# Performance work log

Hardware: AMD Instinct MI355X
Metric: run time of the kernel (lower is better)

Reference implementation:

```python
import jax, jax.numpy as jnp
import numpy as np

LATENT = 3
POLY = 3
SINDY_DIM = 22  # 3 ones + 3 linear + 6 quad + 10 cubic


def sindy_library(z, poly_order=POLY, latent_dim=LATENT):
    # z: [N, latent_dim] -> [N, sindy_dim]; mirrors the torch loop ordering.
    N = z.shape[0]
    cols = [jnp.ones((N,), z.dtype) for _ in range(latent_dim)]
    if poly_order > 0:
        cols += [z[:, i] for i in range(latent_dim)]
    if poly_order > 1:
        for i in range(latent_dim):
            for j in range(i, latent_dim):
                cols.append(z[:, i] * z[:, j])
    if poly_order > 2:
        for i in range(latent_dim):
            for j in range(i, latent_dim):
                for k in range(j, latent_dim):
                    cols.append(z[:, i] * z[:, j] * z[:, k])
    return jnp.stack(cols, axis=1)


def _xavier(key, out_f, in_f):
    lim = np.sqrt(6.0 / (in_f + out_f)).astype(np.float32)
    return jax.random.uniform(key, (out_f, in_f), jnp.float32, -lim, lim)


def setup_inputs() -> dict:
    key = jax.random.key(0)
    ks = jax.random.split(key, 16)
    N, D = 262144, 128
    we = [128, 64, 32, 3]
    wd = [3, 32, 64, 128]
    d = {}
    d["x"] = jax.random.normal(ks[0], (N, D), jnp.float32)
    d["dx"] = jax.random.normal(ks[1], (N, D), jnp.float32)
    for li, (i_f, o_f) in enumerate(zip(we[:-1], we[1:])):
        d[f"We{li+1}"] = _xavier(ks[2 + li], o_f, i_f)
        d[f"be{li+1}"] = jnp.zeros((o_f,), jnp.float32)
    for li, (i_f, o_f) in enumerate(zip(wd[:-1], wd[1:])):
        d[f"Wd{li+1}"] = _xavier(ks[6 + li], o_f, i_f)
        d[f"bd{li+1}"] = jnp.zeros((o_f,), jnp.float32)
    d["EW"] = jnp.full((LATENT, SINDY_DIM), 0.5, jnp.float32)  # nn.init.constant_(E.weight, 0.5)
    d["Eb"] = jax.random.normal(ks[10], (LATENT,), jnp.float32) * 0.1
    return d


def reference(x, dx, We1, be1, We2, be2, We3, be3,
              Wd1, bd1, Wd2, bd2, Wd3, bd3, EW, Eb):
    # encoder forward (Linear + Identity chain)
    z = ((x @ We1.T + be1) @ We2.T + be2) @ We3.T + be3            # [N, L]
    # encoder Jacobian is constant (pure linear chain): J_enc = We3 @ We2 @ We1
    J_enc = We3 @ We2 @ We1                                        # [L, D]
    dz = dx @ J_enc.T                                              # [N, L]
    # SINDy prediction of z-dot
    theta = sindy_library(z)                                       # [N, SINDY_DIM]
    dzb = theta @ EW.T + Eb                                        # [N, L]
    # decoder forward
    xb = ((z @ Wd1.T + bd1) @ Wd2.T + bd2) @ Wd3.T + bd3           # [N, D]
    # decoder Jacobian (constant)
    J_dec = Wd3 @ Wd2 @ Wd1                                        # [D, L]
    dxb = dzb @ J_dec.T                                            # [N, D]
    return z, dz, dzb, xb, dxb
```

## Files before the change

### kernel.cpp

```cpp
#include <hip/hip_runtime.h>

#define D 128

typedef float f32x4 __attribute__((ext_vector_type(4)));

__global__ __launch_bounds__(256) void fuse_weights(
    const float* __restrict__ We1, const float* __restrict__ be1,
    const float* __restrict__ We2, const float* __restrict__ be2,
    const float* __restrict__ We3, const float* __restrict__ be3,
    const float* __restrict__ Wd1, const float* __restrict__ bd1,
    const float* __restrict__ Wd2, const float* __restrict__ bd2,
    const float* __restrict__ Wd3, const float* __restrict__ bd3,
    float* __restrict__ ws)
{
    __shared__ float A1[3][64];
    __shared__ float B1[64][3];
    __shared__ float t2d[64];
    const int t = threadIdx.x;

    if (t < 192) {
        {   int r = t >> 6, c = t & 63;
            float s = 0.f;
            #pragma unroll 8
            for (int i = 0; i < 32; ++i) s += We3[r * 32 + i] * We2[i * 64 + c];
            A1[r][c] = s;
        }
        {   int o = t / 3, l = t - o * 3;
            float s = 0.f;
            #pragma unroll 8
            for (int i = 0; i < 32; ++i) s += Wd2[o * 32 + i] * Wd1[i * 3 + l];
            B1[o][l] = s;
        }
    } else {
        int i = t - 192;
        float s = bd2[i];
        #pragma unroll 8
        for (int j = 0; j < 32; ++j) s += Wd2[i * 32 + j] * bd1[j];
        t2d[i] = s;
    }
    __syncthreads();

    for (int e = t; e < 3 * D; e += 256) {
        int r = e >> 7, c = e & 127;
        float s = 0.f;
        #pragma unroll 8
        for (int j = 0; j < 64; ++j) s += A1[r][j] * We1[j * D + c];
        ws[e] = s;
    }
    if (t < 3) {
        float s = be3[t];
        #pragma unroll 8
        for (int j = 0; j < 64; ++j) s += A1[t][j] * be1[j];
        #pragma unroll 8
        for (int i = 0; i < 32; ++i) s += We3[t * 32 + i] * be2[i];
        ws[384 + t] = s;
    }
    if (t < 128) {
        float s0 = 0.f, s1 = 0.f, s2 = 0.f, sb = bd3[t];
        #pragma unroll 8
        for (int j = 0; j < 64; ++j) {
            float w = Wd3[t * 64 + j];
            s0 += w * B1[j][0];
            s1 += w * B1[j][1];
            s2 += w * B1[j][2];
            sb += w * t2d[j];
        }
        ws[512 + t * 4 + 0] = s0;
        ws[512 + t * 4 + 1] = s1;
        ws[512 + t * 4 + 2] = s2;
        ws[512 + t * 4 + 3] = sb;
    }
}

__global__ __launch_bounds__(256) void enc2(
    const float* __restrict__ x, const float* __restrict__ dx,
    const float* __restrict__ ws, float* __restrict__ zout,
    float* __restrict__ dzout, int nrows)
{
    const int lane = threadIdx.x & 31;
    const int half = threadIdx.x >> 5;

    const f32x4 je0 = *((const f32x4*)(ws + 0 * D) + lane);
    const f32x4 je1 = *((const f32x4*)(ws + 1 * D) + lane);
    const f32x4 je2 = *((const f32x4*)(ws + 2 * D) + lane);
    const float benc0 = ws[384], benc1 = ws[385], benc2 = ws[386];

    const int base = blockIdx.x * 128;

    #pragma unroll 4
    for (int i = 0; i < 16; ++i) {
        const int row = base + i * 8 + half;
        if (row >= nrows) continue;
        const f32x4 xv = __builtin_nontemporal_load((const f32x4*)(x + (size_t)row * D) + lane);
        float z0 = je0.x*xv.x + je0.y*xv.y + je0.z*xv.z + je0.w*xv.w;
        float z1 = je1.x*xv.x + je1.y*xv.y + je1.z*xv.z + je1.w*xv.w;
        float z2 = je2.x*xv.x + je2.y*xv.y + je2.z*xv.z + je2.w*xv.w;
        #pragma unroll
        for (int m = 16; m >= 1; m >>= 1) {
            z0 += __shfl_xor(z0, m);
            z1 += __shfl_xor(z1, m);
            z2 += __shfl_xor(z2, m);
        }
        if (lane < 3) {
            const float zv = (lane == 0) ? z0 + benc0 : (lane == 1) ? z1 + benc1 : z2 + benc2;
            zout[(size_t)row * 3 + lane] = zv;
        }
    }

    __syncthreads();

    #pragma unroll 4
    for (int i = 0; i < 16; ++i) {
        const int row = base + i * 8 + half;
        if (row >= nrows) continue;
        const f32x4 dv = __builtin_nontemporal_load((const f32x4*)(dx + (size_t)row * D) + lane);
        float d0 = je0.x*dv.x + je0.y*dv.y + je0.z*dv.z + je0.w*dv.w;
        float d1 = je1.x*dv.x + je1.y*dv.y + je1.z*dv.z + je1.w*dv.w;
        float d2 = je2.x*dv.x + je2.y*dv.y + je2.z*dv.z + je2.w*dv.w;
        #pragma unroll
        for (int m = 16; m >= 1; m >>= 1) {
            d0 += __shfl_xor(d0, m);
            d1 += __shfl_xor(d1, m);
            d2 += __shfl_xor(d2, m);
        }
        if (lane < 3) {
            const float dvv = (lane == 0) ? d0 : (lane == 1) ? d1 : d2;
            dzout[(size_t)row * 3 + lane] = dvv;
        }
    }
}

__global__ __launch_bounds__(256) void dec2(
    const float* __restrict__ ws, const float* __restrict__ EW,
    const float* __restrict__ Eb, const float* __restrict__ zin,
    float* __restrict__ dzbout, float* __restrict__ xbout,
    float* __restrict__ dxbout, int nrows)
{
    __shared__ float sdzb[384];

    const int lane = threadIdx.x & 31;
    const int half = threadIdx.x >> 5;

    const f32x4 jd0 = *((const f32x4*)(ws + 512) + lane * 4 + 0);
    const f32x4 jd1 = *((const f32x4*)(ws + 512) + lane * 4 + 1);
    const f32x4 jd2 = *((const f32x4*)(ws + 512) + lane * 4 + 2);
    const f32x4 jd3 = *((const f32x4*)(ws + 512) + lane * 4 + 3);

    float ew0[19], ew1[19], ew2[19];
    #pragma unroll
    for (int k = 0; k < 19; ++k) {
        ew0[k] = EW[ 3 + k];
        ew1[k] = EW[25 + k];
        ew2[k] = EW[47 + k];
    }
    const float bs0 = Eb[0] + EW[ 0] + EW[ 1] + EW[ 2];
    const float bs1 = Eb[1] + EW[22] + EW[23] + EW[24];
    const float bs2 = Eb[2] + EW[44] + EW[45] + EW[46];

    const int base = blockIdx.x * 128;

    #pragma unroll 2
    for (int i = 0; i < 16; ++i) {
        const int r2  = i * 8 + half;
        const int row = base + r2;
        if (row >= nrows) continue;

        const float z0 = zin[(size_t)row * 3 + 0];
        const float z1 = zin[(size_t)row * 3 + 1];
        const float z2 = zin[(size_t)row * 3 + 2];

        const float q00 = z0*z0, q01 = z0*z1, q02 = z0*z2;
        const float q11 = z1*z1, q12 = z1*z2, q22 = z2*z2;
        float th[19];
        th[0]=z0;  th[1]=z1;  th[2]=z2;
        th[3]=q00; th[4]=q01; th[5]=q02; th[6]=q11; th[7]=q12; th[8]=q22;
        th[9]=q00*z0;  th[10]=q00*z1; th[11]=q00*z2;
        th[12]=q11*z0; th[13]=q12*z0; th[14]=q22*z0;
        th[15]=q11*z1; th[16]=q11*z2; th[17]=q22*z1; th[18]=q22*z2;

        float b0 = bs0, b1 = bs1, b2 = bs2;
        #pragma unroll
        for (int k = 0; k < 19; ++k) {
            b0 += ew0[k] * th[k];
            b1 += ew1[k] * th[k];
            b2 += ew2[k] * th[k];
        }

        if (lane < 3) {
            const float bv = (lane == 0) ? b0 : (lane == 1) ? b1 : b2;
            dzbout[(size_t)row * 3 + lane] = bv;
            sdzb[r2 * 3 + lane] = bv;
        }

        f32x4 xbv;
        xbv.x = jd0.x*z0 + jd0.y*z1 + jd0.z*z2 + jd0.w;
        xbv.y = jd1.x*z0 + jd1.y*z1 + jd1.z*z2 + jd1.w;
        xbv.z = jd2.x*z0 + jd2.y*z1 + jd2.z*z2 + jd2.w;
        xbv.w = jd3.x*z0 + jd3.y*z1 + jd3.z*z2 + jd3.w;
        __builtin_nontemporal_store(xbv, (f32x4*)(xbout + (size_t)row * D) + lane);
    }

    __syncthreads();

    #pragma unroll 4
    for (int i = 0; i < 16; ++i) {
        const int r2  = i * 8 + half;
        const int row = base + r2;
        if (row >= nrows) continue;

        const float b0 = sdzb[r2 * 3 + 0];
        const float b1 = sdzb[r2 * 3 + 1];
        const float b2 = sdzb[r2 * 3 + 2];

        f32x4 dxbv;
        dxbv.x = jd0.x*b0 + jd0.y*b1 + jd0.z*b2;
        dxbv.y = jd1.x*b0 + jd1.y*b1 + jd1.z*b2;
        dxbv.z = jd2.x*b0 + jd2.y*b1 + jd2.z*b2;
        dxbv.w = jd3.x*b0 + jd3.y*b1 + jd3.z*b2;
        __builtin_nontemporal_store(dxbv, (f32x4*)(dxbout + (size_t)row * D) + lane);
    }
}

extern "C" void kernel_launch(void* const* d_in, const int* in_sizes, int n_in,
                              void* d_out, int out_size, void* d_ws, size_t ws_size,
                              hipStream_t stream) {
    const float* x   = (const float*)d_in[0];
    const float* dx  = (const float*)d_in[1];
    const float* We1 = (const float*)d_in[2];
    const float* be1 = (const float*)d_in[3];
    const float* We2 = (const float*)d_in[4];
    const float* be2 = (const float*)d_in[5];
    const float* We3 = (const float*)d_in[6];
    const float* be3 = (const float*)d_in[7];
    const float* Wd1 = (const float*)d_in[8];
    const float* bd1 = (const float*)d_in[9];
    const float* Wd2 = (const float*)d_in[10];
    const float* bd2 = (const float*)d_in[11];
    const float* Wd3 = (const float*)d_in[12];
    const float* bd3 = (const float*)d_in[13];
    const float* EW  = (const float*)d_in[14];
    const float* Eb  = (const float*)d_in[15];

    float* ws  = (float*)d_ws;
    float* out = (float*)d_out;
    const int nrows = in_sizes[0] / D;
    const int nblk  = (nrows + 127) / 128;

    fuse_weights<<<1, 256, 0, stream>>>(We1, be1, We2, be2, We3, be3,
                                        Wd1, bd1, Wd2, bd2, Wd3, bd3, ws);

    enc2<<<nblk, 256, 0, stream>>>(x, dx, ws,
                                   out,
                                   out + 3 * (size_t)nrows,
                                   nrows);

    dec2<<<nblk, 256, 0, stream>>>(ws, EW, Eb,
                                   out,
                                   out + 6 * (size_t)nrows,
                                   out + 9 * (size_t)nrows,
                                   out + 137 * (size_t)nrows,
                                   nrows);
}
```

Measured before the change: 121.3 us.

## Fuse encoder and decoder kernels into one row-block kernel staging z in LDS

Merges the encoder and decoder kernels into a single kernel that processes 256 rows per block. z, dz and dzb are staged in shared memory and written out with coalesced vector stores. The SINDy polynomial is computed once per row by one thread instead of redundantly across every lane of a wavefront. This removes a kernel launch and the global round trip of z between kernels. In exchange it uses more shared memory per block, has half as many blocks, and puts a serial dependency between the read phase and the write phase inside each block.

```diff
diff --git a/kernel.cpp b/kernel.cpp
--- a/kernel.cpp
+++ b/kernel.cpp
@@ -72,24 +72,39 @@
     }
 }
 
-__global__ __launch_bounds__(256) void enc2(
+__global__ __launch_bounds__(256) void sindy_all(
     const float* __restrict__ x, const float* __restrict__ dx,
-    const float* __restrict__ ws, float* __restrict__ zout,
-    float* __restrict__ dzout, int nrows)
+    const float* __restrict__ EW, const float* __restrict__ Eb,
+    const float* __restrict__ ws, float* __restrict__ out, int nrows)
 {
-    const int lane = threadIdx.x & 31;
-    const int half = threadIdx.x >> 5;
-
-    const f32x4 je0 = *((const f32x4*)(ws + 0 * D) + lane);
-    const f32x4 je1 = *((const f32x4*)(ws + 1 * D) + lane);
-    const f32x4 je2 = *((const f32x4*)(ws + 2 * D) + lane);
+    __shared__ float sz[768];
+    __shared__ float sdz[768];
+    __shared__ float sdzb[768];
+    __shared__ float sew[69];
+
+    const int t    = threadIdx.x;
+    const int lane = t & 31;
+    const int half = t >> 5;
+
+    if (t < 66) sew[t] = EW[t];
+    else if (t < 69) sew[t] = Eb[t - 66];
+
+    const f32x4 je0 = *((const f32x4*)(ws +   0) + lane);
+    const f32x4 je1 = *((const f32x4*)(ws + 128) + lane);
+    const f32x4 je2 = *((const f32x4*)(ws + 256) + lane);
     const float benc0 = ws[384], benc1 = ws[385], benc2 = ws[386];
-
-    const int base = blockIdx.x * 128;
-
-    #pragma unroll 4
-    for (int i = 0; i < 16; ++i) {
-        const int row = base + i * 8 + half;
+    const f32x4 jd0 = *((const f32x4*)(ws + 512) + lane * 4 + 0);
+    const f32x4 jd1 = *((const f32x4*)(ws + 512) + lane * 4 + 1);
+    const f32x4 jd2 = *((const f32x4*)(ws + 512) + lane * 4 + 2);
+    const f32x4 jd3 = *((const f32x4*)(ws + 512) + lane * 4 + 3);
+
+    const int base = blockIdx.x * 256;
+    const int rem  = nrows - base;
+
+    #pragma unroll 4
+    for (int i = 0; i < 32; ++i) {
+        const int r2  = i * 8 + half;
+        const int row = base + r2;
         if (row >= nrows) continue;
         const f32x4 xv = __builtin_nontemporal_load((const f32x4*)(x + (size_t)row * D) + lane);
         float z0 = je0.x*xv.x + je0.y*xv.y + je0.z*xv.z + je0.w*xv.w;
@@ -101,17 +116,17 @@
             z1 += __shfl_xor(z1, m);
             z2 += __shfl_xor(z2, m);
         }
-        if (lane < 3) {
-            const float zv = (lane == 0) ? z0 + benc0 : (lane == 1) ? z1 + benc1 : z2 + benc2;
-            zout[(size_t)row * 3 + lane] = zv;
-        }
-    }
-
-    __syncthreads();
-
-    #pragma unroll 4
-    for (int i = 0; i < 16; ++i) {
-        const int row = base + i * 8 + half;
+        if (lane == 0) {
+            sz[r2 * 3 + 0] = z0 + benc0;
+            sz[r2 * 3 + 1] = z1 + benc1;
+            sz[r2 * 3 + 2] = z2 + benc2;
+        }
+    }
+
+    #pragma unroll 4
+    for (int i = 0; i < 32; ++i) {
+        const int r2  = i * 8 + half;
+        const int row = base + r2;
         if (row >= nrows) continue;
         const f32x4 dv = __builtin_nontemporal_load((const f32x4*)(dx + (size_t)row * D) + lane);
         float d0 = je0.x*dv.x + je0.y*dv.y + je0.z*dv.z + je0.w*dv.w;
@@ -123,51 +138,19 @@
             d1 += __shfl_xor(d1, m);
             d2 += __shfl_xor(d2, m);
         }
-        if (lane < 3) {
-            const float dvv = (lane == 0) ? d0 : (lane == 1) ? d1 : d2;
-            dzout[(size_t)row * 3 + lane] = dvv;
-        }
-    }
-}
-
-__global__ __launch_bounds__(256) void dec2(
-    const float* __restrict__ ws, const float* __restrict__ EW,
-    const float* __restrict__ Eb, const float* __restrict__ zin,
-    float* __restrict__ dzbout, float* __restrict__ xbout,
-    float* __restrict__ dxbout, int nrows)
-{
-    __shared__ float sdzb[384];
-
-    const int lane = threadIdx.x & 31;
-    const int half = threadIdx.x >> 5;
-
-    const f32x4 jd0 = *((const f32x4*)(ws + 512) + lane * 4 + 0);
-    const f32x4 jd1 = *((const f32x4*)(ws + 512) + lane * 4 + 1);
-    const f32x4 jd2 = *((const f32x4*)(ws + 512) + lane * 4 + 2);
-    const f32x4 jd3 = *((const f32x4*)(ws + 512) + lane * 4 + 3);
-
-    float ew0[19], ew1[19], ew2[19];
-    #pragma unroll
-    for (int k = 0; k < 19; ++k) {
-        ew0[k] = EW[ 3 + k];
-        ew1[k] = EW[25 + k];
-        ew2[k] = EW[47 + k];
-    }
-    const float bs0 = Eb[0] + EW[ 0] + EW[ 1] + EW[ 2];
-    const float bs1 = Eb[1] + EW[22] + EW[23] + EW[24];
-    const float bs2 = Eb[2] + EW[44] + EW[45] + EW[46];
-
-    const int base = blockIdx.x * 128;
-
-    #pragma unroll 2
-    for (int i = 0; i < 16; ++i) {
-        const int r2  = i * 8 + half;
-        const int row = base + r2;
-        if (row >= nrows) continue;
-
-        const float z0 = zin[(size_t)row * 3 + 0];
-        const float z1 = zin[(size_t)row * 3 + 1];
-        const float z2 = zin[(size_t)row * 3 + 2];
+        if (lane == 0) {
+            sdz[r2 * 3 + 0] = d0;
+            sdz[r2 * 3 + 1] = d1;
+            sdz[r2 * 3 + 2] = d2;
+        }
+    }
+
+    __syncthreads();
+
+    if (t < rem) {
+        const float z0 = sz[t * 3 + 0];
+        const float z1 = sz[t * 3 + 1];
+        const float z2 = sz[t * 3 + 2];
 
         const float q00 = z0*z0, q01 = z0*z1, q02 = z0*z2;
         const float q11 = z1*z1, q12 = z1*z2, q22 = z2*z2;
@@ -178,46 +161,68 @@
         th[12]=q11*z0; th[13]=q12*z0; th[14]=q22*z0;
         th[15]=q11*z1; th[16]=q11*z2; th[17]=q22*z1; th[18]=q22*z2;
 
-        float b0 = bs0, b1 = bs1, b2 = bs2;
+        float b0 = sew[66] + sew[0]  + sew[1]  + sew[2];
+        float b1 = sew[67] + sew[22] + sew[23] + sew[24];
+        float b2 = sew[68] + sew[44] + sew[45] + sew[46];
         #pragma unroll
         for (int k = 0; k < 19; ++k) {
-            b0 += ew0[k] * th[k];
-            b1 += ew1[k] * th[k];
-            b2 += ew2[k] * th[k];
-        }
-
-        if (lane < 3) {
-            const float bv = (lane == 0) ? b0 : (lane == 1) ? b1 : b2;
-            dzbout[(size_t)row * 3 + lane] = bv;
-            sdzb[r2 * 3 + lane] = bv;
-        }
-
-        f32x4 xbv;
-        xbv.x = jd0.x*z0 + jd0.y*z1 + jd0.z*z2 + jd0.w;
-        xbv.y = jd1.x*z0 + jd1.y*z1 + jd1.z*z2 + jd1.w;
-        xbv.z = jd2.x*z0 + jd2.y*z1 + jd2.z*z2 + jd2.w;
-        xbv.w = jd3.x*z0 + jd3.y*z1 + jd3.z*z2 + jd3.w;
-        __builtin_nontemporal_store(xbv, (f32x4*)(xbout + (size_t)row * D) + lane);
+            b0 += sew[3  + k] * th[k];
+            b1 += sew[25 + k] * th[k];
+            b2 += sew[47 + k] * th[k];
+        }
+        sdzb[t * 3 + 0] = b0;
+        sdzb[t * 3 + 1] = b1;
+        sdzb[t * 3 + 2] = b2;
     }
 
     __syncthreads();
 
-    #pragma unroll 4
-    for (int i = 0; i < 16; ++i) {
-        const int r2  = i * 8 + half;
-        const int row = base + r2;
-        if (row >= nrows) continue;
-
+    if (rem >= 256) {
+        if (t < 192) {
+            ((f32x4*)(out + (size_t)base * 3))[t]                    = ((const f32x4*)sz)[t];
+            ((f32x4*)(out + 3 * (size_t)nrows + (size_t)base * 3))[t] = ((const f32x4*)sdz)[t];
+            ((f32x4*)(out + 6 * (size_t)nrows + (size_t)base * 3))[t] = ((const f32x4*)sdzb)[t];
+        }
+    } else {
+        for (int e = t; e < rem * 3; e += 256) {
+            out[(size_t)base * 3 + e]                     = sz[e];
+            out[3 * (size_t)nrows + (size_t)base * 3 + e] = sdz[e];
+            out[6 * (size_t)nrows + (size_t)base * 3 + e] = sdzb[e];
+        }
+    }
+
+    float* __restrict__ xbout = out + 9 * (size_t)nrows;
+    #pragma unroll 4
+    for (int i = 0; i < 32; ++i) {
+        const int r2  = i * 8 + half;
+        const int row = base + r2;
+        if (row >= nrows) continue;
+        const float z0 = sz[r2 * 3 + 0];
+        const float z1 = sz[r2 * 3 + 1];
+        const float z2 = sz[r2 * 3 + 2];
+        f32x4 v;
+        v.x = jd0.x*z0 + jd0.y*z1 + jd0.z*z2 + jd0.w;
+        v.y = jd1.x*z0 + jd1.y*z1 + jd1.z*z2 + jd1.w;
+        v.z = jd2.x*z0 + jd2.y*z1 + jd2.z*z2 + jd2.w;
+        v.w = jd3.x*z0 + jd3.y*z1 + jd3.z*z2 + jd3.w;
+        __builtin_nontemporal_store(v, (f32x4*)(xbout + (size_t)row * D) + lane);
+    }
+
+    float* __restrict__ dxbout = out + 137 * (size_t)nrows;
+    #pragma unroll 4
+    for (int i = 0; i < 32; ++i) {
+        const int r2  = i * 8 + half;
+        const int row = base + r2;
+        if (row >= nrows) continue;
         const float b0 = sdzb[r2 * 3 + 0];
         const float b1 = sdzb[r2 * 3 + 1];
         const float b2 = sdzb[r2 * 3 + 2];
-
-        f32x4 dxbv;
-        dxbv.x = jd0.x*b0 + jd0.y*b1 + jd0.z*b2;
-        dxbv.y = jd1.x*b0 + jd1.y*b1 + jd1.z*b2;
-        dxbv.z = jd2.x*b0 + jd2.y*b1 + jd2.z*b2;
-        dxbv.w = jd3.x*b0 + jd3.y*b1 + jd3.z*b2;
-        __builtin_nontemporal_store(dxbv, (f32x4*)(dxbout + (size_t)row * D) + lane);
+        f32x4 v;
+        v.x = jd0.x*b0 + jd0.y*b1 + jd0.z*b2;
+        v.y = jd1.x*b0 + jd1.y*b1 + jd1.z*b2;
+        v.z = jd2.x*b0 + jd2.y*b1 + jd2.z*b2;
+        v.w = jd3.x*b0 + jd3.y*b1 + jd3.z*b2;
+        __builtin_nontemporal_store(v, (f32x4*)(dxbout + (size_t)row * D) + lane);
     }
 }
 
@@ -244,20 +249,10 @@
     float* ws  = (float*)d_ws;
     float* out = (float*)d_out;
     const int nrows = in_sizes[0] / D;
-    const int nblk  = (nrows + 127) / 128;
+    const int nblk  = (nrows + 255) / 256;
 
     fuse_weights<<<1, 256, 0, stream>>>(We1, be1, We2, be2, We3, be3,
                                         Wd1, bd1, Wd2, bd2, Wd3, bd3, ws);
 
-    enc2<<<nblk, 256, 0, stream>>>(x, dx, ws,
-                                   out,
-                                   out + 3 * (size_t)nrows,
-                                   nrows);
-
-    dec2<<<nblk, 256, 0, stream>>>(ws, EW, Eb,
-                                   out,
-                                   out + 6 * (size_t)nrows,
-                                   out + 9 * (size_t)nrows,
-                                   out + 137 * (size_t)nrows,
-                                   nrows);
+    sindy_all<<<nblk, 256, 0, stream>>>(x, dx, EW, Eb, ws, out, nrows);
 }
```

After: 124.6 us. 1.03x slower.
